# Kernel tuning notes

Hardware: AMD Instinct MI355X
Metric: run time of the kernel (lower is better)

The kernel has to match this reference:

```python
import jax, jax.numpy as jnp
import numpy as np

B, S, D, H = 2, 2048, 1024, 16
HD = D // H  # head_dim = 64


def setup_inputs() -> dict:
    key = jax.random.key(0)
    k1, k2, k3 = jax.random.split(key, 3)
    x = jax.random.normal(k1, (B, S, D), dtype=jnp.float32)
    W_qkv = jax.random.normal(k2, (D, 3 * D), dtype=jnp.float32) * (D ** -0.5)
    b_qkv = jnp.zeros((3 * D,), dtype=jnp.float32)
    W_proj = jax.random.normal(k3, (D, D), dtype=jnp.float32) * (D ** -0.5)
    b_proj = jnp.zeros((D,), dtype=jnp.float32)
    return {"x": x, "W_qkv": W_qkv, "b_qkv": b_qkv, "W_proj": W_proj, "b_proj": b_proj}


def reference(x, W_qkv, b_qkv, W_proj, b_proj):
    b, s, d = x.shape
    scale = HD ** -0.5
    qkv = x @ W_qkv + b_qkv                       # [B,S,3D]
    q, k, v = jnp.split(qkv, 3, axis=-1)
    # [B,S,D] -> [B,H,S,HD]
    def to_heads(t):
        return t.reshape(b, s, H, HD).transpose(0, 2, 1, 3)
    q, k, v = map(to_heads, (q, k, v))
    scores = jnp.einsum('bhqd,bhkd->bhqk', q, k) * scale  # [B,H,S,S]
    causal = jnp.triu(jnp.ones((s, s), dtype=bool), k=1)
    scores = jnp.where(causal[None, None], -jnp.inf, scores)
    attn = jax.nn.softmax(scores, axis=-1)
    out = jnp.einsum('bhqk,bhkd->bhqd', attn, v)  # [B,H,S,HD]
    out = out.transpose(0, 2, 1, 3).reshape(b, s, d)
    return out @ W_proj + b_proj
```

## Files before the change

### kernel.cpp

```cpp
#include <hip/hip_runtime.h>

using frag_t = __attribute__((ext_vector_type(8))) short;
using f32x4  = __attribute__((ext_vector_type(4))) float;

#define L2E 1.4426950408889634f

#if __has_builtin(__builtin_amdgcn_exp2f)
#define EXP2(x) __builtin_amdgcn_exp2f(x)
#else
#define EXP2(x) exp2f(x)
#endif

constexpr int B_  = 2, S_ = 2048, D_ = 1024, H_ = 16, HD_ = 64;
constexpr int M_  = B_ * S_;
constexpr float QSCALE = 0.125f * L2E;

__device__ __forceinline__ ushort f2bf(float f) {
  union { float f; unsigned u; } v; v.f = f;
  unsigned u = v.u;
  unsigned r = (u + 0x7FFFu + ((u >> 16) & 1u)) >> 16;
  return (ushort)r;
}

__device__ __forceinline__ void gld_lds16(const ushort* g, ushort* l) {
  __builtin_amdgcn_global_load_lds((const __attribute__((address_space(1))) void*)g,
                                   (__attribute__((address_space(3))) void*)l, 16, 0, 0);
}

__global__ __launch_bounds__(256) void k_prep(
    const float* __restrict__ x, const float* __restrict__ Wqkv,
    const float* __restrict__ Wproj,
    ushort* __restrict__ Xbf, ushort* __restrict__ Wqt, ushort* __restrict__ Wpt) {
  int blk = blockIdx.x, tid = threadIdx.x;
  if (blk < 1024) {
    size_t base = (size_t)blk * 4096 + tid * 4;
    #pragma unroll
    for (int i = 0; i < 4; ++i) {
      float4 f = *(const float4*)(x + base + i * 1024);
      ushort4 o;
      o.x = f2bf(f.x); o.y = f2bf(f.y); o.z = f2bf(f.z); o.w = f2bf(f.w);
      *(ushort4*)(Xbf + base + i * 1024) = o;
    }
  } else {
    __shared__ float tile[64][65];
    const float* in; ushort* out; int N, K, bx, by;
    if (blk < 1024 + 768) { int b2 = blk - 1024; in = Wqkv;  out = Wqt; N = 3072; K = 1024; bx = b2 % 48; by = b2 / 48; }
    else                  { int b2 = blk - 1792; in = Wproj; out = Wpt; N = 1024; K = 1024; bx = b2 % 16; by = b2 / 16; }
    int n0 = bx * 64, k0 = by * 64;
    int tx = tid & 63, ty = tid >> 6;
    #pragma unroll
    for (int i = 0; i < 16; ++i)
      tile[ty + i * 4][tx] = in[(size_t)(k0 + ty + i * 4) * N + n0 + tx];
    __syncthreads();
    #pragma unroll
    for (int i = 0; i < 16; ++i)
      out[(size_t)(n0 + ty + i * 4) * K + k0 + tx] = f2bf(tile[tx][ty + i * 4]);
  }
}

__global__ __launch_bounds__(512, 2) void k_gemm8(
    const ushort* __restrict__ A, const ushort* __restrict__ Bt,
    const float* __restrict__ bias,
    ushort* __restrict__ Qo, ushort* __restrict__ Ko, ushort* __restrict__ Vo) {
  __shared__ ushort smem[65536];
  int tid = threadIdx.x;
  int lane = tid & 63, wave = tid >> 6;
  int quad = lane >> 4, li = lane & 15;
  int wm = wave >> 2, wn = wave & 3;
  int wg = blockIdx.x;
  int swz = (wg & 7) * 24 + (wg >> 3);
  int by = swz / 12, bx = swz % 12;
  int m0 = by * 256, n0 = bx * 256;
  const ushort* Asrc = A  + (size_t)m0 * 1024;
  const ushort* Bsrc = Bt + (size_t)n0 * 1024;
  int srow   = lane >> 2;
  int schunk = (lane & 3) ^ ((lane >> 4) & 3);
  int pos    = (quad ^ ((li >> 2) & 3)) * 8;

#define STG(BI, ISB, KS, KT) do { \
    const ushort* _s = (ISB) ? Bsrc : Asrc; \
    ushort* _d = &smem[((BI)*4 + (ISB)*2 + (KS)) * 8192]; \
    _Pragma("unroll") \
    for (int j = 0; j < 2; ++j) \
      gld_lds16(&_s[(size_t)(j*128 + wave*16 + srow) * 1024 + (KT)*64 + (KS)*32 + schunk*8], \
                &_d[(j*128 + wave*16) * 32]); \
  } while (0)

  f32x4 acc[8][4] = {};
  frag_t af[8], bf[2];

#define PH(BI, KS, NH, STGS, W4) do { \
    if ((NH) == 0) { \
      _Pragma("unroll") \
      for (int mi = 0; mi < 8; ++mi) \
        af[mi] = *(const frag_t*)&smem[((BI)*4 + (KS)) * 8192 + (wm*128 + mi*16 + li) * 32 + pos]; \
    } \
    _Pragma("unroll") \
    for (int nj = 0; nj < 2; ++nj) \
      bf[nj] = *(const frag_t*)&smem[((BI)*4 + 2 + (KS)) * 8192 + (wn*64 + ((NH)*2 + nj)*16 + li) * 32 + pos]; \
    STGS; \
    if (W4) asm volatile("s_waitcnt vmcnt(4)" ::: "memory"); \
    asm volatile("s_barrier" ::: "memory"); \
    __builtin_amdgcn_s_setprio(1); \
    _Pragma("unroll") \
    for (int mi = 0; mi < 8; ++mi) { \
      acc[mi][(NH)*2+0] = __builtin_amdgcn_mfma_f32_16x16x32_bf16(af[mi], bf[0], acc[mi][(NH)*2+0], 0, 0, 0); \
      acc[mi][(NH)*2+1] = __builtin_amdgcn_mfma_f32_16x16x32_bf16(af[mi], bf[1], acc[mi][(NH)*2+1], 0, 0, 0); \
    } \
    __builtin_amdgcn_s_setprio(0); \
    asm volatile("s_barrier" ::: "memory"); \
  } while (0)

  STG(0,0,0,0); STG(0,1,0,0); STG(0,0,1,0); STG(0,1,1,0);
  STG(1,0,0,1); STG(1,1,0,1);
  asm volatile("s_waitcnt vmcnt(4)" ::: "memory");
  asm volatile("s_barrier" ::: "memory");

  for (int it = 0; it < 8; ++it) {
    int t1 = 2*it + 1;
    int t2 = (2*it + 2 < 16) ? 2*it + 2 : 15;
    int t3 = (2*it + 3 < 16) ? 2*it + 3 : 15;
    PH(0,0,0, STG(1,0,1,t1), 0);
    PH(0,0,1, STG(1,1,1,t1), 0);
    PH(0,1,0, STG(0,0,0,t2), 0);
    PH(0,1,1, STG(0,1,0,t2), 1);
    PH(1,0,0, STG(0,0,1,t2), 0);
    PH(1,0,1, STG(0,1,1,t2), 0);
    PH(1,1,0, STG(1,0,0,t3), 0);
    PH(1,1,1, STG(1,1,0,t3), 1);
  }
#undef PH
#undef STG

  asm volatile("s_waitcnt vmcnt(0)" ::: "memory");
  __syncthreads();

  int which = (n0 + wn * 64) >> 10;
  if (which < 2) {
    #pragma unroll
    for (int ni = 0; ni < 4; ++ni) {
      int gcol = n0 + wn * 64 + ni * 16 + li;
      float bv = bias[gcol];
      int d = gcol & 1023, h = d >> 6, hd = d & 63;
      #pragma unroll
      for (int mi = 0; mi < 8; ++mi)
        #pragma unroll
        for (int r = 0; r < 4; ++r) {
          int grow = m0 + wm * 128 + mi * 16 + quad * 4 + r;
          int b = grow >> 11, s = grow & 2047;
          size_t off = (((size_t)b * H_ + h) * S_ + s) * HD_ + hd;
          float v = acc[mi][ni][r] + bv;
          if (which == 0) Qo[off] = f2bf(v * QSCALE);
          else            Ko[off] = f2bf(v);
        }
    }
  } else {
    ushort* vl = &smem[wave * 8192];
    #pragma unroll
    for (int ni = 0; ni < 4; ++ni) {
      int row = ni * 16 + li;
      float bv = bias[n0 + wn * 64 + row];
      int rx = (row & 7) << 3;
      #pragma unroll
      for (int mi = 0; mi < 8; ++mi) {
        int g  = (mi & 1) * 4 + quad;
        int gm = g & 3;
        int gp = (gm == 1 || gm == 2) ? (g ^ 3) : g;
        #pragma unroll
        for (int r = 0; r < 4; ++r) {
          int col = (mi >> 1) * 32 + gp * 4 + r;
          vl[row * 128 + (col ^ rx)] = f2bf(acc[mi][ni][r] + bv);
        }
      }
    }
    int h  = ((n0 & 1023) + wn * 64) >> 6;
    int b  = m0 >> 11;
    int s0 = (m0 & 2047) + wm * 128;
    size_t vbase = ((size_t)b * H_ + h) * HD_ * S_;
    #pragma unroll
    for (int i = 0; i < 16; ++i) {
      int row = i * 4 + quad;
      int col = li * 8;
      *(uint4*)&Vo[vbase + (size_t)row * S_ + s0 + col] =
          *(const uint4*)&vl[row * 128 + (col ^ ((row & 7) << 3))];
    }
  }
}

template <int EPI>
__global__ __launch_bounds__(256) void k_gemm(
    const ushort* __restrict__ A, const ushort* __restrict__ Bt,
    const float* __restrict__ bias,
    float* __restrict__ Co, int N, int K) {
  constexpr int BM = 64;
  constexpr int BN = 64, BK = 64;
  constexpr int MI = 2, NI = 2;
  __shared__ ushort smem[(BM + BN) * BK];
  ushort* As = smem;
  ushort* Bs = smem + BM * BK;
  int tid  = threadIdx.x;
  int lane = tid & 63, wave = tid >> 6;
  int quad = lane >> 4, li = lane & 15;
  int mbase = (wave >> 1) * (MI * 16);
  int nbase = (wave & 1) * 32;
  int m0 = blockIdx.y * BM, n0 = blockIdx.x * BN;
  int srow = lane >> 3;
  int scol = ((lane & 7) ^ srow) * 8;
  f32x4 acc[MI][NI] = {};
  for (int k0 = 0; k0 < K; k0 += BK) {
    #pragma unroll
    for (int i = 0; i < 2; ++i) {
      int rbase = wave * 16 + i * 8;
      gld_lds16(&A[(size_t)(m0 + rbase + srow) * K + k0 + scol], &As[rbase * BK]);
    }
    #pragma unroll
    for (int i = 0; i < 2; ++i) {
      int rbase = wave * 16 + i * 8;
      gld_lds16(&Bt[(size_t)(n0 + rbase + srow) * K + k0 + scol], &Bs[rbase * BK]);
    }
    __syncthreads();
    #pragma unroll
    for (int ks = 0; ks < 2; ++ks) {
      frag_t af[MI], bf[NI];
      #pragma unroll
      for (int mi = 0; mi < MI; ++mi)
        af[mi] = *(const frag_t*)&As[(mbase + mi * 16 + li) * BK + (((ks * 4 + quad) ^ (li & 7)) * 8)];
      #pragma unroll
      for (int ni = 0; ni < NI; ++ni)
        bf[ni] = *(const frag_t*)&Bs[(nbase + ni * 16 + li) * BK + (((ks * 4 + quad) ^ (li & 7)) * 8)];
      #pragma unroll
      for (int mi = 0; mi < MI; ++mi)
        #pragma unroll
        for (int ni = 0; ni < NI; ++ni)
          acc[mi][ni] = __builtin_amdgcn_mfma_f32_16x16x32_bf16(af[mi], bf[ni], acc[mi][ni], 0, 0, 0);
    }
    __syncthreads();
  }
  #pragma unroll
  for (int mi = 0; mi < MI; ++mi)
    #pragma unroll
    for (int ni = 0; ni < NI; ++ni) {
      int gcol = n0 + nbase + ni * 16 + li;
      float bv = bias[gcol];
      #pragma unroll
      for (int r = 0; r < 4; ++r) {
        int grow = m0 + mbase + mi * 16 + quad * 4 + r;
        Co[(size_t)grow * N + gcol] = acc[mi][ni][r] + bv;
      }
    }
}

__global__ __launch_bounds__(256) void k_attn(
    const ushort* __restrict__ Q, const ushort* __restrict__ K,
    const ushort* __restrict__ Vt, ushort* __restrict__ O) {
  __shared__ ushort Kbuf[2][64 * 64];
  __shared__ ushort Vbuf[2][64 * 64];
  int lane = threadIdx.x & 63, wave = threadIdx.x >> 6;
  int quad = lane >> 4, li = lane & 15;
  int bh = blockIdx.x;
  int qb = 31 - (int)blockIdx.y;
  int b = bh >> 4, hh = bh & 15;
  int q0 = qb * 64 + wave * 16;
  const ushort* Qb = Q  + (size_t)bh * S_ * HD_;
  const ushort* Kb = K  + (size_t)bh * S_ * HD_;
  const ushort* Vb = Vt + (size_t)bh * HD_ * S_;

  frag_t qf[2];
  #pragma unroll
  for (int ks = 0; ks < 2; ++ks)
    qf[ks] = *(const frag_t*)&Qb[(size_t)(q0 + li) * HD_ + ks * 32 + quad * 8];

  frag_t ones;
  #pragma unroll
  for (int i = 0; i < 8; ++i) ones[i] = (short)0x3F80;

  f32x4 o[4] = {};
  f32x4 lacc = {};

  auto stage = [&](int kb, int bi) {
    #pragma unroll
    for (int i = 0; i < 2; ++i) {
      int rt  = wave * 16 + i * 8 + (lane >> 3);
      int c16 = (lane & 7) ^ (lane >> 3);
      gld_lds16(&Kb[(size_t)(kb * 64 + rt) * HD_ + c16 * 8], &Kbuf[bi][(wave * 16 + i * 8) * 64]);
      gld_lds16(&Vb[(size_t)rt * S_ + kb * 64 + c16 * 8],    &Vbuf[bi][(wave * 16 + i * 8) * 64]);
    }
  };

  auto comp = [&](int kb, bool diag, int bi) {
    f32x4 sc[4];
    #pragma unroll
    for (int t = 0; t < 4; ++t) {
      f32x4 a = {};
      #pragma unroll
      for (int ks = 0; ks < 2; ++ks) {
        frag_t kf = *(const frag_t*)&Kbuf[bi][(t * 16 + li) * 64 + (((quad + ks * 4) ^ (li & 7)) * 8)];
        a = __builtin_amdgcn_mfma_f32_16x16x32_bf16(kf, qf[ks], a, 0, 0, 0);
      }
      sc[t] = a;
    }
    if (diag) {
      #pragma unroll
      for (int t = 0; t < 4; ++t) {
        int key = kb * 64 + t * 16 + quad * 4;
        #pragma unroll
        for (int r = 0; r < 4; ++r)
          if (key + r > q0 + li) sc[t][r] = -1e30f;
      }
    }
    #pragma unroll
    for (int t = 0; t < 4; ++t)
      #pragma unroll
      for (int r = 0; r < 4; ++r)
        sc[t][r] = EXP2(sc[t][r]);

    frag_t pf[2];
    #pragma unroll
    for (int ks = 0; ks < 2; ++ks) {
      unsigned w0e, w1e, w0o, w1o;
      asm("v_cvt_pk_bf16_f32 %0, %1, %2" : "=v"(w0e) : "v"(sc[2*ks][0]),   "v"(sc[2*ks][1]));
      asm("v_cvt_pk_bf16_f32 %0, %1, %2" : "=v"(w1e) : "v"(sc[2*ks][2]),   "v"(sc[2*ks][3]));
      asm("v_cvt_pk_bf16_f32 %0, %1, %2" : "=v"(w0o) : "v"(sc[2*ks+1][0]), "v"(sc[2*ks+1][1]));
      asm("v_cvt_pk_bf16_f32 %0, %1, %2" : "=v"(w1o) : "v"(sc[2*ks+1][2]), "v"(sc[2*ks+1][3]));
      asm("v_permlane32_swap_b32 %0, %1" : "+v"(w0e), "+v"(w0o));
      asm("v_permlane32_swap_b32 %0, %1" : "+v"(w1e), "+v"(w1o));
      union { frag_t f; unsigned u[4]; } pu;
      pu.u[0] = w0e; pu.u[1] = w1e; pu.u[2] = w0o; pu.u[3] = w1o;
      pf[ks] = pu.f;
    }
    lacc = __builtin_amdgcn_mfma_f32_16x16x32_bf16(ones, pf[0], lacc, 0, 0, 0);
    lacc = __builtin_amdgcn_mfma_f32_16x16x32_bf16(ones, pf[1], lacc, 0, 0, 0);
    #pragma unroll
    for (int ht = 0; ht < 4; ++ht)
      #pragma unroll
      for (int ks = 0; ks < 2; ++ks) {
        frag_t vtf = *(const frag_t*)&Vbuf[bi][(ht * 16 + li) * 64 + (((ks * 4 + quad) ^ (li & 7)) * 8)];
        o[ht] = __builtin_amdgcn_mfma_f32_16x16x32_bf16(vtf, pf[ks], o[ht], 0, 0, 0);
      }
  };

  stage(0, 0);
  __syncthreads();
  for (int kb = 0; kb <= qb; ++kb) {
    if (kb < qb) stage(kb + 1, (kb + 1) & 1);
    comp(kb, kb == qb, kb & 1);
    __syncthreads();
  }

  float inv = 1.f / lacc[0];
  int srow = q0 + li;
  size_t obase = ((size_t)b * S_ + srow) * D_ + hh * 64 + quad * 4;
  #pragma unroll
  for (int ht = 0; ht < 4; ++ht) {
    unsigned lo, hi;
    asm("v_cvt_pk_bf16_f32 %0, %1, %2" : "=v"(lo) : "v"(o[ht][0] * inv), "v"(o[ht][1] * inv));
    asm("v_cvt_pk_bf16_f32 %0, %1, %2" : "=v"(hi) : "v"(o[ht][2] * inv), "v"(o[ht][3] * inv));
    uint2 w; w.x = lo; w.y = hi;
    *(uint2*)&O[obase + ht * 16] = w;
  }
}

extern "C" void kernel_launch(void* const* d_in, const int* in_sizes, int n_in,
                              void* d_out, int out_size, void* d_ws, size_t ws_size,
                              hipStream_t stream) {
  (void)in_sizes; (void)n_in; (void)out_size; (void)ws_size;
  const float* x     = (const float*)d_in[0];
  const float* Wqkv  = (const float*)d_in[1];
  const float* bqkv  = (const float*)d_in[2];
  const float* Wproj = (const float*)d_in[3];
  const float* bproj = (const float*)d_in[4];
  float* out = (float*)d_out;

  char* ws = (char*)d_ws;
  ushort* Xbf = (ushort*)(ws);
  ushort* Wqt = (ushort*)(ws + (8u  << 20));
  ushort* Wpt = (ushort*)(ws + (14u << 20));
  ushort* Qbf = (ushort*)(ws + (16u << 20));
  ushort* Kbf = (ushort*)(ws + (24u << 20));
  ushort* Vtb = (ushort*)(ws + (32u << 20));
  ushort* Obf = Xbf;

  k_prep<<<dim3(2048), dim3(256), 0, stream>>>(x, Wqkv, Wproj, Xbf, Wqt, Wpt);
  k_gemm8<<<dim3(192), dim3(512), 0, stream>>>(Xbf, Wqt, bqkv, Qbf, Kbf, Vtb);
  k_attn<<<dim3(B_ * H_, 32), dim3(256), 0, stream>>>(Qbf, Kbf, Vtb, Obf);
  k_gemm<1><<<dim3(16, 64), dim3(256), 0, stream>>>(Obf, Wpt, bproj, out, D_, D_);
}
```

Baseline: 169.4 us.

## Split attention key blocks across waves with LDS merge; enlarge projection GEMM tile

The attention kernel no longer has each wave own 16 query rows while streaming K/V through double-buffered LDS. Each wave now handles all 64 query rows of the tile over an interleaved subset of key blocks, loading K and V fragments straight from global memory. The waves' partial outputs and row sums are then reduced through shared memory. This removes per-block barriers and LDS staging in the main loop, and each K/V fragment is reused across four query groups. The cost is more registers, uncoalesced global fragment loads, and a serialized four-step merge epilogue. Separately, the output projection GEMM becomes a specialized kernel with 128-row tiles and half as many blocks.

New measurement: 179.9 us. +6.2%, slower.

```diff
diff --git a/kernel.cpp b/kernel.cpp
--- a/kernel.cpp
+++ b/kernel.cpp
@@ -187,14 +187,11 @@
   }
 }
 
-template <int EPI>
-__global__ __launch_bounds__(256) void k_gemm(
+__global__ __launch_bounds__(256) void k_proj(
     const ushort* __restrict__ A, const ushort* __restrict__ Bt,
-    const float* __restrict__ bias,
-    float* __restrict__ Co, int N, int K) {
-  constexpr int BM = 64;
-  constexpr int BN = 64, BK = 64;
-  constexpr int MI = 2, NI = 2;
+    const float* __restrict__ bias, float* __restrict__ Co) {
+  constexpr int BM = 128, BN = 64, BK = 64, MI = 4, NI = 2;
+  constexpr int N = 1024, K = 1024;
   __shared__ ushort smem[(BM + BN) * BK];
   ushort* As = smem;
   ushort* Bs = smem + BM * BK;
@@ -209,8 +206,8 @@
   f32x4 acc[MI][NI] = {};
   for (int k0 = 0; k0 < K; k0 += BK) {
     #pragma unroll
-    for (int i = 0; i < 2; ++i) {
-      int rbase = wave * 16 + i * 8;
+    for (int i = 0; i < 4; ++i) {
+      int rbase = i * 32 + wave * 8;
       gld_lds16(&A[(size_t)(m0 + rbase + srow) * K + k0 + scol], &As[rbase * BK]);
     }
     #pragma unroll
@@ -253,110 +250,119 @@
 __global__ __launch_bounds__(256) void k_attn(
     const ushort* __restrict__ Q, const ushort* __restrict__ K,
     const ushort* __restrict__ Vt, ushort* __restrict__ O) {
-  __shared__ ushort Kbuf[2][64 * 64];
-  __shared__ ushort Vbuf[2][64 * 64];
+  __shared__ float mrg[4][64][21];
   int lane = threadIdx.x & 63, wave = threadIdx.x >> 6;
   int quad = lane >> 4, li = lane & 15;
   int bh = blockIdx.x;
-  int qb = 31 - (int)blockIdx.y;
+  int qt = 31 - (int)blockIdx.y;
   int b = bh >> 4, hh = bh & 15;
-  int q0 = qb * 64 + wave * 16;
+  int q0 = qt * 64;
   const ushort* Qb = Q  + (size_t)bh * S_ * HD_;
   const ushort* Kb = K  + (size_t)bh * S_ * HD_;
   const ushort* Vb = Vt + (size_t)bh * HD_ * S_;
 
-  frag_t qf[2];
+  frag_t qf[4][2];
   #pragma unroll
-  for (int ks = 0; ks < 2; ++ks)
-    qf[ks] = *(const frag_t*)&Qb[(size_t)(q0 + li) * HD_ + ks * 32 + quad * 8];
+  for (int qg = 0; qg < 4; ++qg)
+    #pragma unroll
+    for (int ks = 0; ks < 2; ++ks)
+      qf[qg][ks] = *(const frag_t*)&Qb[(size_t)(q0 + qg * 16 + li) * HD_ + ks * 32 + quad * 8];
 
   frag_t ones;
   #pragma unroll
   for (int i = 0; i < 8; ++i) ones[i] = (short)0x3F80;
 
-  f32x4 o[4] = {};
-  f32x4 lacc = {};
-
-  auto stage = [&](int kb, int bi) {
-    #pragma unroll
-    for (int i = 0; i < 2; ++i) {
-      int rt  = wave * 16 + i * 8 + (lane >> 3);
-      int c16 = (lane & 7) ^ (lane >> 3);
-      gld_lds16(&Kb[(size_t)(kb * 64 + rt) * HD_ + c16 * 8], &Kbuf[bi][(wave * 16 + i * 8) * 64]);
-      gld_lds16(&Vb[(size_t)rt * S_ + kb * 64 + c16 * 8],    &Vbuf[bi][(wave * 16 + i * 8) * 64]);
-    }
-  };
-
-  auto comp = [&](int kb, bool diag, int bi) {
-    f32x4 sc[4];
-    #pragma unroll
-    for (int t = 0; t < 4; ++t) {
-      f32x4 a = {};
+  f32x4 o[4][4] = {};
+  f32x4 lacc[4] = {};
+
+  for (int kb = wave; kb <= qt; kb += 4) {
+    bool diag = (kb == qt);
+    frag_t kf[4][2];
+    #pragma unroll
+    for (int t = 0; t < 4; ++t)
+      #pragma unroll
+      for (int ks = 0; ks < 2; ++ks)
+        kf[t][ks] = *(const frag_t*)&Kb[(size_t)(kb * 64 + t * 16 + li) * HD_ + (ks * 4 + quad) * 8];
+
+    frag_t pf[4][2];
+    #pragma unroll
+    for (int qg = 0; qg < 4; ++qg) {
+      f32x4 sc[4];
+      #pragma unroll
+      for (int t = 0; t < 4; ++t) {
+        f32x4 a = {};
+        a = __builtin_amdgcn_mfma_f32_16x16x32_bf16(kf[t][0], qf[qg][0], a, 0, 0, 0);
+        a = __builtin_amdgcn_mfma_f32_16x16x32_bf16(kf[t][1], qf[qg][1], a, 0, 0, 0);
+        sc[t] = a;
+      }
+      if (diag) {
+        #pragma unroll
+        for (int t = 0; t < 4; ++t) {
+          int key = kb * 64 + t * 16 + quad * 4;
+          #pragma unroll
+          for (int r = 0; r < 4; ++r)
+            if (key + r > q0 + qg * 16 + li) sc[t][r] = -1e30f;
+        }
+      }
+      #pragma unroll
+      for (int t = 0; t < 4; ++t)
+        #pragma unroll
+        for (int r = 0; r < 4; ++r)
+          sc[t][r] = EXP2(sc[t][r]);
       #pragma unroll
       for (int ks = 0; ks < 2; ++ks) {
-        frag_t kf = *(const frag_t*)&Kbuf[bi][(t * 16 + li) * 64 + (((quad + ks * 4) ^ (li & 7)) * 8)];
-        a = __builtin_amdgcn_mfma_f32_16x16x32_bf16(kf, qf[ks], a, 0, 0, 0);
-      }
-      sc[t] = a;
-    }
-    if (diag) {
-      #pragma unroll
-      for (int t = 0; t < 4; ++t) {
-        int key = kb * 64 + t * 16 + quad * 4;
-        #pragma unroll
-        for (int r = 0; r < 4; ++r)
-          if (key + r > q0 + li) sc[t][r] = -1e30f;
-      }
-    }
-    #pragma unroll
-    for (int t = 0; t < 4; ++t)
+        unsigned w0e, w1e, w0o, w1o;
+        asm("v_cvt_pk_bf16_f32 %0, %1, %2" : "=v"(w0e) : "v"(sc[2*ks][0]),   "v"(sc[2*ks][1]));
+        asm("v_cvt_pk_bf16_f32 %0, %1, %2" : "=v"(w1e) : "v"(sc[2*ks][2]),   "v"(sc[2*ks][3]));
+        asm("v_cvt_pk_bf16_f32 %0, %1, %2" : "=v"(w0o) : "v"(sc[2*ks+1][0]), "v"(sc[2*ks+1][1]));
+        asm("v_cvt_pk_bf16_f32 %0, %1, %2" : "=v"(w1o) : "v"(sc[2*ks+1][2]), "v"(sc[2*ks+1][3]));
+        asm("v_permlane32_swap_b32 %0, %1" : "+v"(w0e), "+v"(w0o));
+        asm("v_permlane32_swap_b32 %0, %1" : "+v"(w1e), "+v"(w1o));
+        union { frag_t f; unsigned u[4]; } pu;
+        pu.u[0] = w0e; pu.u[1] = w1e; pu.u[2] = w0o; pu.u[3] = w1o;
+        pf[qg][ks] = pu.f;
+      }
+      lacc[qg] = __builtin_amdgcn_mfma_f32_16x16x32_bf16(ones, pf[qg][0], lacc[qg], 0, 0, 0);
+      lacc[qg] = __builtin_amdgcn_mfma_f32_16x16x32_bf16(ones, pf[qg][1], lacc[qg], 0, 0, 0);
+    }
+    #pragma unroll
+    for (int ht = 0; ht < 4; ++ht)
+      #pragma unroll
+      for (int ks = 0; ks < 2; ++ks) {
+        frag_t vtf = *(const frag_t*)&Vb[(size_t)(ht * 16 + li) * S_ + kb * 64 + (ks * 4 + quad) * 8];
+        #pragma unroll
+        for (int qg = 0; qg < 4; ++qg)
+          o[qg][ht] = __builtin_amdgcn_mfma_f32_16x16x32_bf16(vtf, pf[qg][ks], o[qg][ht], 0, 0, 0);
+      }
+  }
+
+  #pragma unroll
+  for (int qg = 0; qg < 4; ++qg) {
+    #pragma unroll
+    for (int ht = 0; ht < 4; ++ht)
       #pragma unroll
       for (int r = 0; r < 4; ++r)
-        sc[t][r] = EXP2(sc[t][r]);
-
-    frag_t pf[2];
-    #pragma unroll
-    for (int ks = 0; ks < 2; ++ks) {
-      unsigned w0e, w1e, w0o, w1o;
-      asm("v_cvt_pk_bf16_f32 %0, %1, %2" : "=v"(w0e) : "v"(sc[2*ks][0]),   "v"(sc[2*ks][1]));
-      asm("v_cvt_pk_bf16_f32 %0, %1, %2" : "=v"(w1e) : "v"(sc[2*ks][2]),   "v"(sc[2*ks][3]));
-      asm("v_cvt_pk_bf16_f32 %0, %1, %2" : "=v"(w0o) : "v"(sc[2*ks+1][0]), "v"(sc[2*ks+1][1]));
-      asm("v_cvt_pk_bf16_f32 %0, %1, %2" : "=v"(w1o) : "v"(sc[2*ks+1][2]), "v"(sc[2*ks+1][3]));
-      asm("v_permlane32_swap_b32 %0, %1" : "+v"(w0e), "+v"(w0o));
-      asm("v_permlane32_swap_b32 %0, %1" : "+v"(w1e), "+v"(w1o));
-      union { frag_t f; unsigned u[4]; } pu;
-      pu.u[0] = w0e; pu.u[1] = w1e; pu.u[2] = w0o; pu.u[3] = w1o;
-      pf[ks] = pu.f;
-    }
-    lacc = __builtin_amdgcn_mfma_f32_16x16x32_bf16(ones, pf[0], lacc, 0, 0, 0);
-    lacc = __builtin_amdgcn_mfma_f32_16x16x32_bf16(ones, pf[1], lacc, 0, 0, 0);
-    #pragma unroll
-    for (int ht = 0; ht < 4; ++ht)
-      #pragma unroll
-      for (int ks = 0; ks < 2; ++ks) {
-        frag_t vtf = *(const frag_t*)&Vbuf[bi][(ht * 16 + li) * 64 + (((ks * 4 + quad) ^ (li & 7)) * 8)];
-        o[ht] = __builtin_amdgcn_mfma_f32_16x16x32_bf16(vtf, pf[ks], o[ht], 0, 0, 0);
-      }
-  };
-
-  stage(0, 0);
-  __syncthreads();
-  for (int kb = 0; kb <= qb; ++kb) {
-    if (kb < qb) stage(kb + 1, (kb + 1) & 1);
-    comp(kb, kb == qb, kb & 1);
-    __syncthreads();
-  }
-
-  float inv = 1.f / lacc[0];
-  int srow = q0 + li;
-  size_t obase = ((size_t)b * S_ + srow) * D_ + hh * 64 + quad * 4;
-  #pragma unroll
-  for (int ht = 0; ht < 4; ++ht) {
-    unsigned lo, hi;
-    asm("v_cvt_pk_bf16_f32 %0, %1, %2" : "=v"(lo) : "v"(o[ht][0] * inv), "v"(o[ht][1] * inv));
-    asm("v_cvt_pk_bf16_f32 %0, %1, %2" : "=v"(hi) : "v"(o[ht][2] * inv), "v"(o[ht][3] * inv));
-    uint2 w; w.x = lo; w.y = hi;
-    *(uint2*)&O[obase + ht * 16] = w;
+        mrg[wave][lane][ht * 4 + r] = o[qg][ht][r];
+    mrg[wave][lane][16] = lacc[qg][0];
+    __syncthreads();
+    if (wave == qg) {
+      float s17[17];
+      #pragma unroll
+      for (int j = 0; j < 17; ++j)
+        s17[j] = mrg[0][lane][j] + mrg[1][lane][j] + mrg[2][lane][j] + mrg[3][lane][j];
+      float inv = 1.f / s17[16];
+      int srow = q0 + qg * 16 + li;
+      size_t obase = ((size_t)b * S_ + srow) * D_ + hh * 64 + quad * 4;
+      #pragma unroll
+      for (int ht = 0; ht < 4; ++ht) {
+        unsigned lo, hi;
+        asm("v_cvt_pk_bf16_f32 %0, %1, %2" : "=v"(lo) : "v"(s17[ht*4+0] * inv), "v"(s17[ht*4+1] * inv));
+        asm("v_cvt_pk_bf16_f32 %0, %1, %2" : "=v"(hi) : "v"(s17[ht*4+2] * inv), "v"(s17[ht*4+3] * inv));
+        uint2 w; w.x = lo; w.y = hi;
+        *(uint2*)&O[obase + ht * 16] = w;
+      }
+    }
+    __syncthreads();
   }
 }
 
@@ -383,5 +389,5 @@
   k_prep<<<dim3(2048), dim3(256), 0, stream>>>(x, Wqkv, Wproj, Xbf, Wqt, Wpt);
   k_gemm8<<<dim3(192), dim3(512), 0, stream>>>(Xbf, Wqt, bqkv, Qbf, Kbf, Vtb);
   k_attn<<<dim3(B_ * H_, 32), dim3(256), 0, stream>>>(Qbf, Kbf, Vtb, Obf);
-  k_gemm<1><<<dim3(16, 64), dim3(256), 0, stream>>>(Obf, Wpt, bproj, out, D_, D_);
-}
+  k_proj<<<dim3(16, 32), dim3(256), 0, stream>>>(Obf, Wpt, bproj, out);
+}
```
